# Optimization experiments

Measured on AMD Instinct MI355X. Metric: run time of the kernel, lower is better.

The kernel has to match this reference:

```python
import jax, jax.numpy as jnp
import numpy as np

MAX_PATH_DISTANCE = 5
NUM_HEADS = 4
BATCH_SIZE = 64
MAX_NODES = 512
EDGES_PER_GRAPH = 16384


def setup_inputs() -> dict:
    rng = np.random.default_rng(0)
    # deterministic variable graph sizes in {512, 448, 384, 320}; max is 512
    n = (MAX_NODES - (np.arange(BATCH_SIZE) % 4) * 64).astype(np.int64)
    offsets = np.concatenate([[0], np.cumsum(n)[:-1]])
    batch = np.repeat(np.arange(BATCH_SIZE, dtype=np.int64), n)  # [total_nodes]
    g = np.repeat(np.arange(BATCH_SIZE, dtype=np.int64), EDGES_PER_GRAPH)
    src_local = rng.integers(0, n[g])
    dst_local = rng.integers(0, n[g])
    edge_index = np.stack([src_local + offsets[g], dst_local + offsets[g]]).astype(np.int64)
    key = jax.random.key(0)
    edge_bias_weight = jax.random.normal(key, (MAX_PATH_DISTANCE + 2, NUM_HEADS), dtype=jnp.float32)
    return {
        "edge_index": jnp.asarray(edge_index),
        "batch": jnp.asarray(batch),
        "num_nodes_per_graph": jnp.asarray(n),
        "edge_bias_weight": edge_bias_weight,
    }


def reference(edge_index, batch, num_nodes_per_graph, edge_bias_weight):
    B = num_nodes_per_graph.shape[0]
    N = MAX_NODES  # == num_nodes_per_graph.max()
    K = MAX_PATH_DISTANCE
    # per-graph node offsets -> local node ids
    offsets = jnp.concatenate(
        [jnp.zeros((1,), num_nodes_per_graph.dtype), jnp.cumsum(num_nodes_per_graph)[:-1]]
    )
    g = batch[edge_index[0]]  # graph id per edge
    si = edge_index[0] - offsets[g]
    di = edge_index[1] - offsets[g]
    # dense adjacency per graph (to_dense_adj equivalent)
    adj = jnp.zeros((B, N, N), dtype=bool).at[g, si, di].set(True)
    # validity mask: node index < n_b
    valid = jnp.arange(N)[None, :] < num_nodes_per_graph[:, None]  # [B, N]
    pair = valid[:, :, None] & valid[:, None, :]  # [B, N, N]
    # distance: 1 where edge (inside n x n block), else K+1; diagonal of block = 0
    dist = jnp.where(adj & pair, 1, K + 1)
    eye = jnp.eye(N, dtype=bool)[None]
    dist = jnp.where(eye & pair, 0, dist)  # values already within [0, K+1], no clamp needed
    bias = edge_bias_weight[dist]  # [B, N, N, H] embedding gather
    return jnp.transpose(bias, (0, 3, 1, 2))  # [B, H, N, N]
```

## Files before the change

### kernel.cpp

```cpp
#include <hip/hip_runtime.h>
#include <hip/hip_bf16.h>
#include <stdint.h>

#define NGRAPH 64
#define NMAX   512
#define NHEAD  4
#define ROWS_PER_BLOCK 64
#define SLICES (NMAX / ROWS_PER_BLOCK)
#define NBLOCKS (NGRAPH * SLICES)

typedef float f4 __attribute__((ext_vector_type(4)));

__global__ __launch_bounds__(256) void fused_structenc_kernel(
    const int* __restrict__ ei,
    const int* __restrict__ nn,
    const float* __restrict__ W,
    f4* __restrict__ out4,
    int E, int epg)
{
    int cpx = NBLOCKS >> 3;
    int wg  = (blockIdx.x & 7) * cpx + (blockIdx.x >> 3);
    int g     = wg >> 3;
    int slice = wg & 7;
    int r0    = slice * ROWS_PER_BLOCK;

    __shared__ uint32_t s_bits[ROWS_PER_BLOCK * (NMAX / 32)];
    __shared__ int s_off;

    int t = threadIdx.x;
#pragma unroll
    for (int z = 0; z < 4; ++z) s_bits[t + z * 256] = 0u;

    if (t < 64) {
        int v = nn[t];
        int x = v;
#pragma unroll
        for (int d = 1; d < 64; d <<= 1) {
            int y = __shfl_up(x, d, 64);
            if (t >= d) x += y;
        }
        if (t == g) s_off = x - v;
    }
    __syncthreads();

    int off   = s_off;
    int ebase = g * epg;
    {
        const int4* src4 = reinterpret_cast<const int4*>(ei + ebase);
        int nvec = epg >> 2;
        for (int idx = t; idx < nvec; idx += 256) {
            int4 s = src4[idx];
            int e0 = ebase + (idx << 2);
#pragma unroll
            for (int c = 0; c < 4; ++c) {
                int si = ((const int*)&s)[c] - off;
                unsigned rr = (unsigned)(si - r0);
                if (rr < (unsigned)ROWS_PER_BLOCK) {
                    int di = ei[E + e0 + c] - off;
                    atomicOr(&s_bits[rr * 16 + (di >> 5)], 1u << (di & 31));
                }
            }
        }
        for (int k = (nvec << 2) + t; k < epg; k += 256) {
            int si = ei[ebase + k] - off;
            unsigned rr = (unsigned)(si - r0);
            if (rr < (unsigned)ROWS_PER_BLOCK) {
                int di = ei[E + ebase + k] - off;
                atomicOr(&s_bits[rr * 16 + (di >> 5)], 1u << (di & 31));
            }
        }
    }
    __syncthreads();

    int lane = t & 63;
    int h    = t >> 6;
    int nb   = nn[g];
    float w0 = W[h];
    float w1 = W[4 + h];
    float w6 = W[24 + h];
    size_t outbase = ((size_t)(g * NHEAD + h) * NMAX + r0) * (NMAX / 4);

    int j0 = lane << 2;
#pragma unroll 8
    for (int r = 0; r < ROWS_PER_BLOCK; ++r) {
        int i = r0 + r;
        uint32_t blo = s_bits[r * 16 +     (lane >> 3)] >> ((lane & 7) << 2);
        uint32_t bhi = s_bits[r * 16 + 8 + (lane >> 3)] >> ((lane & 7) << 2);
        f4 lo, hi;
        bool dv = (i < nb);
#pragma unroll
        for (int k2 = 0; k2 < 4; ++k2) {
            float v = ((blo >> k2) & 1u) ? w1 : w6;
            if (dv && (j0 + k2) == i) v = w0;
            lo[k2] = v;
            float v2 = ((bhi >> k2) & 1u) ? w1 : w6;
            if (dv && (256 + j0 + k2) == i) v2 = w0;
            hi[k2] = v2;
        }
        __builtin_nontemporal_store(lo, &out4[outbase + (size_t)r * 128 + lane]);
        __builtin_nontemporal_store(hi, &out4[outbase + (size_t)r * 128 + 64 + lane]);
    }
}

extern "C" void kernel_launch(void* const* d_in, const int* in_sizes, int n_in,
                              void* d_out, int out_size, void* d_ws, size_t ws_size,
                              hipStream_t stream) {
    const int*   ei = (const int*)d_in[0];
    const int*   nn = (const int*)d_in[2];
    const float* W  = (const float*)d_in[3];
    f4* out4 = (f4*)d_out;

    int E   = in_sizes[0] / 2;
    int epg = E / NGRAPH;

    fused_structenc_kernel<<<NBLOCKS, 256, 0, stream>>>(ei, nn, W, out4, E, epg);
}
```

Measured before the change: 62.84 us.

## Split fused kernel into zero, global-bitmap scan, and write kernels

Replaces the single fused kernel with three launches: zero a global adjacency bitmap in workspace and compute per-graph offsets, scan every edge exactly once with global atomicOr, then write the output two rows per wavefront from the bitmap. This removes the redundant edge rescans, since each of the 8 row-slice blocks per graph previously read all of that graph's edges. In exchange it adds two extra launches, a 2 MB global bitmap round trip, and global atomics. The old fused kernel is kept as a fallback when the workspace is too small.

```diff
diff --git a/kernel.cpp b/kernel.cpp
--- a/kernel.cpp
+++ b/kernel.cpp
@@ -5,33 +5,18 @@
 #define NGRAPH 64
 #define NMAX   512
 #define NHEAD  4
-#define ROWS_PER_BLOCK 64
-#define SLICES (NMAX / ROWS_PER_BLOCK)
-#define NBLOCKS (NGRAPH * SLICES)
+#define BITMAP_WORDS (NGRAPH * NMAX * (NMAX / 32))
+#define BITMAP_BYTES (BITMAP_WORDS * 4)
 
 typedef float f4 __attribute__((ext_vector_type(4)));
 
-__global__ __launch_bounds__(256) void fused_structenc_kernel(
-    const int* __restrict__ ei,
-    const int* __restrict__ nn,
-    const float* __restrict__ W,
-    f4* __restrict__ out4,
-    int E, int epg)
-{
-    int cpx = NBLOCKS >> 3;
-    int wg  = (blockIdx.x & 7) * cpx + (blockIdx.x >> 3);
-    int g     = wg >> 3;
-    int slice = wg & 7;
-    int r0    = slice * ROWS_PER_BLOCK;
-
-    __shared__ uint32_t s_bits[ROWS_PER_BLOCK * (NMAX / 32)];
-    __shared__ int s_off;
-
-    int t = threadIdx.x;
-#pragma unroll
-    for (int z = 0; z < 4; ++z) s_bits[t + z * 256] = 0u;
-
-    if (t < 64) {
+__global__ void zero_prep_kernel(uint4* __restrict__ bm4,
+                                 const int* __restrict__ nn,
+                                 int* __restrict__ offs) {
+    int tid = blockIdx.x * blockDim.x + threadIdx.x;
+    bm4[tid] = make_uint4(0u, 0u, 0u, 0u);
+    if (blockIdx.x == 0 && threadIdx.x < 64) {
+        int t = threadIdx.x;
         int v = nn[t];
         int x = v;
 #pragma unroll
@@ -39,47 +24,130 @@
             int y = __shfl_up(x, d, 64);
             if (t >= d) x += y;
         }
+        offs[t] = x - v;
+    }
+}
+
+__global__ void scan_kernel(const int* __restrict__ ei,
+                            const int* __restrict__ offs,
+                            uint32_t* __restrict__ bm,
+                            int E, int epg) {
+    int idx = blockIdx.x * blockDim.x + threadIdx.x;
+    const int4* src4 = reinterpret_cast<const int4*>(ei);
+    const int4* dst4 = reinterpret_cast<const int4*>(ei + E);
+    int4 s = src4[idx];
+    int4 d = dst4[idx];
+    int e0 = idx << 2;
+    int g  = e0 / epg;
+    int off = offs[g];
+    int base = g * (NMAX * NMAX / 32);
+#pragma unroll
+    for (int c = 0; c < 4; ++c) {
+        int si = ((const int*)&s)[c] - off;
+        int di = ((const int*)&d)[c] - off;
+        atomicOr(&bm[base + si * 16 + (di >> 5)], 1u << (di & 31));
+    }
+}
+
+__global__ void write_kernel(const uint32_t* __restrict__ bm,
+                             const int* __restrict__ nn,
+                             const float* __restrict__ W,
+                             f4* __restrict__ out4) {
+    int tid  = blockIdx.x * blockDim.x + threadIdx.x;
+    int lane = tid & 63;
+    int R    = (tid >> 6) << 1;
+    int i    = R & 511;
+    int h    = (R >> 9) & 3;
+    int b    = R >> 11;
+
+    int nb = nn[b];
+    float w0 = W[h];
+    float w1 = W[4 + h];
+    float w6 = W[24 + h];
+
+    const uint32_t* row = bm + ((b << 9) + i) * 16;
+    int wq = lane >> 3;
+    int sh = (lane & 7) << 2;
+    uint32_t b00 = row[wq]      >> sh;
+    uint32_t b01 = row[8 + wq]  >> sh;
+    uint32_t b10 = row[16 + wq] >> sh;
+    uint32_t b11 = row[24 + wq] >> sh;
+
+    int j0 = lane << 2;
+    f4 v0, v1, v2, v3;
+    bool dv0 = (i < nb);
+    bool dv1 = (i + 1 < nb);
+#pragma unroll
+    for (int k = 0; k < 4; ++k) {
+        int j = j0 + k;
+        float x0 = ((b00 >> k) & 1u) ? w1 : w6;
+        if (dv0 && j == i) x0 = w0;
+        v0[k] = x0;
+        float x1 = ((b01 >> k) & 1u) ? w1 : w6;
+        if (dv0 && (256 + j) == i) x1 = w0;
+        v1[k] = x1;
+        float x2 = ((b10 >> k) & 1u) ? w1 : w6;
+        if (dv1 && j == i + 1) x2 = w0;
+        v2[k] = x2;
+        float x3 = ((b11 >> k) & 1u) ? w1 : w6;
+        if (dv1 && (256 + j) == i + 1) x3 = w0;
+        v3[k] = x3;
+    }
+    size_t base = (size_t)R << 7;
+    __builtin_nontemporal_store(v0, &out4[base + lane]);
+    __builtin_nontemporal_store(v1, &out4[base + 64 + lane]);
+    __builtin_nontemporal_store(v2, &out4[base + 128 + lane]);
+    __builtin_nontemporal_store(v3, &out4[base + 192 + lane]);
+}
+
+#define ROWS_PER_BLOCK 64
+#define SLICES (NMAX / ROWS_PER_BLOCK)
+#define NBLOCKS (NGRAPH * SLICES)
+
+__global__ __launch_bounds__(256) void fused_structenc_kernel(
+    const int* __restrict__ ei, const int* __restrict__ nn,
+    const float* __restrict__ W, f4* __restrict__ out4, int E, int epg)
+{
+    int cpx = NBLOCKS >> 3;
+    int wg  = (blockIdx.x & 7) * cpx + (blockIdx.x >> 3);
+    int g     = wg >> 3;
+    int slice = wg & 7;
+    int r0    = slice * ROWS_PER_BLOCK;
+    __shared__ uint32_t s_bits[ROWS_PER_BLOCK * (NMAX / 32)];
+    __shared__ int s_off;
+    int t = threadIdx.x;
+#pragma unroll
+    for (int z = 0; z < 4; ++z) s_bits[t + z * 256] = 0u;
+    if (t < 64) {
+        int v = nn[t]; int x = v;
+#pragma unroll
+        for (int d = 1; d < 64; d <<= 1) { int y = __shfl_up(x, d, 64); if (t >= d) x += y; }
         if (t == g) s_off = x - v;
     }
     __syncthreads();
-
-    int off   = s_off;
+    int off = s_off;
     int ebase = g * epg;
-    {
-        const int4* src4 = reinterpret_cast<const int4*>(ei + ebase);
-        int nvec = epg >> 2;
-        for (int idx = t; idx < nvec; idx += 256) {
-            int4 s = src4[idx];
-            int e0 = ebase + (idx << 2);
+    const int4* src4 = reinterpret_cast<const int4*>(ei + ebase);
+    int nvec = epg >> 2;
+    for (int idx = t; idx < nvec; idx += 256) {
+        int4 s = src4[idx];
+        int e0 = ebase + (idx << 2);
 #pragma unroll
-            for (int c = 0; c < 4; ++c) {
-                int si = ((const int*)&s)[c] - off;
-                unsigned rr = (unsigned)(si - r0);
-                if (rr < (unsigned)ROWS_PER_BLOCK) {
-                    int di = ei[E + e0 + c] - off;
-                    atomicOr(&s_bits[rr * 16 + (di >> 5)], 1u << (di & 31));
-                }
-            }
-        }
-        for (int k = (nvec << 2) + t; k < epg; k += 256) {
-            int si = ei[ebase + k] - off;
+        for (int c = 0; c < 4; ++c) {
+            int si = ((const int*)&s)[c] - off;
             unsigned rr = (unsigned)(si - r0);
             if (rr < (unsigned)ROWS_PER_BLOCK) {
-                int di = ei[E + ebase + k] - off;
+                int di = ei[E + e0 + c] - off;
                 atomicOr(&s_bits[rr * 16 + (di >> 5)], 1u << (di & 31));
             }
         }
     }
     __syncthreads();
-
     int lane = t & 63;
     int h    = t >> 6;
     int nb   = nn[g];
-    float w0 = W[h];
-    float w1 = W[4 + h];
-    float w6 = W[24 + h];
+    float w0 = W[h], w1 = W[4 + h], w6 = W[24 + h];
     size_t outbase = ((size_t)(g * NHEAD + h) * NMAX + r0) * (NMAX / 4);
-
     int j0 = lane << 2;
 #pragma unroll 8
     for (int r = 0; r < ROWS_PER_BLOCK; ++r) {
@@ -113,5 +181,15 @@
     int E   = in_sizes[0] / 2;
     int epg = E / NGRAPH;
 
-    fused_structenc_kernel<<<NBLOCKS, 256, 0, stream>>>(ei, nn, W, out4, E, epg);
+    size_t need = (size_t)BITMAP_BYTES + NGRAPH * sizeof(int);
+    if (ws_size >= need) {
+        uint32_t* bm = (uint32_t*)d_ws;
+        int* offs = (int*)((char*)d_ws + BITMAP_BYTES);
+        zero_prep_kernel<<<BITMAP_BYTES / 16 / 256, 256, 0, stream>>>((uint4*)d_ws, nn, offs);
+        scan_kernel<<<(E / 4) / 256, 256, 0, stream>>>(ei, offs, bm, E, epg);
+        int wthreads = out_size / 16;
+        write_kernel<<<wthreads / 256, 256, 0, stream>>>(bm, nn, W, out4);
+    } else {
+        fused_structenc_kernel<<<NBLOCKS, 256, 0, stream>>>(ei, nn, W, out4, E, epg);
+    }
 }
```

After: 100.9 us. 1.61x slower.
